# Kernel tuning notes

Measured on AMD Instinct MI355X. Metric: run time of the kernel, lower is better.

The kernel has to match this reference:

```python
import jax, jax.numpy as jnp
import numpy as np

NUM_LEVELS = 8
BASE_RES = 32
MAX_RES = 2048
FEAT_DIM = 8
MAX_TABLE = 2 ** 19
WIDTH = 256
DEPTH = 8
NUM_FREQS = 4
N = 1048576

RESOLUTIONS = [min(BASE_RES * 2 ** l, MAX_RES) for l in range(NUM_LEVELS)]
TABLE_SIZES = [min(r ** 3, MAX_TABLE) for r in RESOLUTIONS]
POS_DIM = NUM_LEVELS * FEAT_DIM            # 64
VIEW_DIM = 3 + 3 * 2 * NUM_FREQS          # 27
IN_DIM = POS_DIM + VIEW_DIM                # 91


def _xavier(key, shape):
    fan_in, fan_out = shape[-2], shape[-1]
    limit = float(np.sqrt(6.0 / (fan_in + fan_out)))
    return jax.random.uniform(key, shape, jnp.float32, -limit, limit)


def setup_inputs() -> dict:
    key = jax.random.key(0)
    ks = jax.random.split(key, 32)
    inp = {
        'positions': jax.random.uniform(ks[0], (N, 3), jnp.float32),  # in [0,1) subset of [-1,1]
        'viewdirs': jax.random.normal(ks[1], (N, 3), jnp.float32),
    }
    for l in range(NUM_LEVELS):
        inp[f'table{l}'] = _xavier(ks[2 + l], (TABLE_SIZES[l], FEAT_DIM))
    inp['w0'] = _xavier(ks[12], (IN_DIM, WIDTH))
    inp['b0'] = jnp.zeros((WIDTH,), jnp.float32)
    # 6 hidden (with ReLU) + 1 final (no ReLU) 256x256 linears, stacked
    inp['wh'] = _xavier(ks[13], (DEPTH - 1, WIDTH, WIDTH))
    inp['bh'] = jnp.zeros((DEPTH - 1, WIDTH), jnp.float32)
    inp['wd'] = _xavier(ks[14], (WIDTH, 1))
    inp['bd'] = jnp.zeros((1,), jnp.float32)
    inp['wc'] = _xavier(ks[15], (WIDTH, 3))
    inp['bc'] = jnp.zeros((3,), jnp.float32)
    return inp


def _hash_encode(positions, table, res):
    # (p + 1) * 0.5 * res, clamped to [0, res-1]
    ps = jnp.clip((positions + 1.0) * (0.5 * res), 0.0, res - 1.0)
    idx_f = ps[..., 0] * (res * res) + ps[..., 1] * res + ps[..., 2]
    # clamp in float first so int32 cast is safe (matches torch clamp-to-table)
    idx = jnp.clip(idx_f, 0.0, table.shape[0] - 1.0).astype(jnp.int32)
    return table[idx]  # [..., FEAT_DIM]


def _view_encode(v):
    feats = [v]
    for f in range(NUM_FREQS):
        feats.append(jnp.sin((2.0 ** f) * jnp.pi * v))
        feats.append(jnp.cos((2.0 ** f) * jnp.pi * v))
    return jnp.concatenate(feats, axis=-1)


def reference(positions, viewdirs, table0, table1, table2, table3, table4,
              table5, table6, table7, w0, b0, wh, bh, wd, bd, wc, bc):
    tables = [table0, table1, table2, table3, table4, table5, table6, table7]
    spatial = jnp.concatenate(
        [_hash_encode(positions, tables[l], RESOLUTIONS[l]) for l in range(NUM_LEVELS)],
        axis=-1)                                           # [N, 64]
    feats = jnp.concatenate([spatial, _view_encode(viewdirs)], axis=-1)  # [N, 91]

    x = jax.nn.relu(feats @ w0 + b0)
    for i in range(DEPTH - 2):                             # 6 hidden layers with ReLU
        x = jax.nn.relu(x @ wh[i] + bh[i])
    x = x @ wh[DEPTH - 2] + bh[DEPTH - 2]                  # final linear, no ReLU

    density = x @ wd + bd                                  # [N, 1]
    color = jax.nn.sigmoid(x @ wc + bc)                    # [N, 3]
    return density, color
```

## Files before the change

### kernel.cpp

```cpp
#include <hip/hip_runtime.h>
#include <math.h>

#define N_PTS 1048576

typedef _Float16 half8 __attribute__((ext_vector_type(8)));
typedef _Float16 half4v __attribute__((ext_vector_type(4)));
typedef float float4v __attribute__((ext_vector_type(4)));
typedef float f32x16 __attribute__((ext_vector_type(16)));

#define W0T_OFF 0
#define WHT_OFF 24576
#define WHEAD_OFF 483328
#define WS_HALVES 487424

__global__ void prep_weights(const float* __restrict__ w0,
                             const float* __restrict__ wh,
                             const float* __restrict__ wd,
                             const float* __restrict__ wc,
                             _Float16* __restrict__ ws) {
  int stride = gridDim.x * blockDim.x;
  for (int i = blockIdx.x * blockDim.x + threadIdx.x; i < WS_HALVES; i += stride) {
    float v;
    if (i < WHT_OFF) {
      int kb = i >> 11, n = (i >> 3) & 255, j = i & 7;
      int k = kb * 8 + j;
      v = (k < 91) ? w0[k * 256 + n] : 0.0f;
    } else if (i < WHEAD_OFF) {
      int rel = i - WHT_OFF;
      int layer = rel >> 16;
      int r = rel & 65535;
      int kb = r >> 11, n = (r >> 3) & 255, j = r & 7;
      int k = kb * 8 + j;
      v = wh[(layer << 16) + k * 256 + n];
    } else {
      int rel = i - WHEAD_OFF;
      int n = rel >> 8, k = rel & 255;
      v = (n == 0) ? wd[k] : ((n < 4) ? wc[k * 3 + n - 1] : 0.0f);
    }
    ws[i] = (_Float16)v;
  }
}

__device__ __forceinline__ int xaddr(int m, int kb) {
  return m * 512 + (kb ^ ((m & 7) << 4));
}

template <int KB>
__device__ __forceinline__ void mlp_layer(char* X, const _Float16* __restrict__ Wt,
                                          const float* __restrict__ bias, bool relu,
                                          int w, int lr5, int lg2) {
  f32x16 acc[4];
#pragma unroll
  for (int mt = 0; mt < 4; ++mt)
#pragma unroll
    for (int r = 0; r < 16; ++r) acc[mt][r] = 0.0f;

  const _Float16* wbase = Wt + ((size_t)(lg2 * 256 + w * 32 + lr5)) * 8;
  const int swz = (lr5 & 7) << 4;
  const int cbase = lg2 * 16;

  half8 a_cur = *(const half8*)wbase;
#pragma unroll
  for (int ks = 0; ks < KB; ++ks) {
    half8 a_nxt = a_cur;
    if (ks + 1 < KB) a_nxt = *(const half8*)(wbase + (size_t)(ks + 1) * 4096);
    const int c = (ks * 32 + cbase) ^ swz;
#pragma unroll
    for (int mt = 0; mt < 4; ++mt) {
      half8 b = *(const half8*)&X[(mt * 32 + lr5) * 512 + c];
      acc[mt] = __builtin_amdgcn_mfma_f32_32x32x16_f16(a_cur, b, acc[mt], 0, 0, 0);
    }
    a_cur = a_nxt;
  }
  __syncthreads();

  const float* bptr = bias + w * 32 + lg2 * 4;
  float4v bq[4];
#pragma unroll
  for (int q = 0; q < 4; ++q) bq[q] = *(const float4v*)(bptr + q * 8);
#pragma unroll
  for (int mt = 0; mt < 4; ++mt) {
    const int rowb = (mt * 32 + lr5) * 512;
#pragma unroll
    for (int q = 0; q < 4; ++q) {
      half4v hv;
#pragma unroll
      for (int rr = 0; rr < 4; ++rr) {
        float y = acc[mt][q * 4 + rr] + bq[q][rr];
        if (relu) y = fmaxf(y, 0.0f);
        hv[rr] = (_Float16)y;
      }
      *(half4v*)&X[rowb + ((w * 64 + q * 16 + lg2 * 8) ^ swz)] = hv;
    }
  }
  __syncthreads();
}

__global__ __launch_bounds__(512, 4) void nerf_fused(
    const float* __restrict__ pos, const float* __restrict__ vdir,
    const float* __restrict__ t0, const float* __restrict__ t1,
    const float* __restrict__ t2, const float* __restrict__ t3,
    const float* __restrict__ t4, const float* __restrict__ t5,
    const float* __restrict__ t6, const float* __restrict__ t7,
    const float* __restrict__ b0, const float* __restrict__ bh,
    const float* __restrict__ bd, const float* __restrict__ bc,
    const _Float16* __restrict__ ws, float* __restrict__ out) {
  __shared__ __align__(16) char X[65536];
  const int tid = threadIdx.x;
  const int wg = blockIdx.x;
  const int m = tid & 127;
  const int part = tid >> 7;
  const int p = wg * 128 + m;

  if (part < 3) {
    const float px = pos[p * 3], py = pos[p * 3 + 1], pz = pos[p * 3 + 2];
    const float* tabs[8] = {t0, t1, t2, t3, t4, t5, t6, t7};
    const int resi[8] = {32, 64, 128, 256, 512, 1024, 2048, 2048};
    const float tmax[8] = {32767.0f, 262143.0f, 524287.0f, 524287.0f,
                           524287.0f, 524287.0f, 524287.0f, 524287.0f};
    const int lv0 = part * 3;
    const int lv1 = (part == 2) ? 8 : lv0 + 3;
    for (int lv = lv0; lv < lv1; ++lv) {
      const float r = (float)resi[lv];
      const float hr = 0.5f * r;
      const float rm1 = r - 1.0f;
      float cx = fminf(fmaxf(__fmul_rn(__fadd_rn(px, 1.0f), hr), 0.0f), rm1);
      float cy = fminf(fmaxf(__fmul_rn(__fadd_rn(py, 1.0f), hr), 0.0f), rm1);
      float cz = fminf(fmaxf(__fmul_rn(__fadd_rn(pz, 1.0f), hr), 0.0f), rm1);
      float idxf = __fadd_rn(__fadd_rn(__fmul_rn(cx, r * r), __fmul_rn(cy, r)), cz);
      idxf = fminf(fmaxf(idxf, 0.0f), tmax[lv]);
      int idx = (int)idxf;
      const float4* row = (const float4*)(tabs[lv] + (size_t)idx * 8);
      float4 f0 = row[0], f1 = row[1];
      half8 h;
      h[0] = (_Float16)f0.x; h[1] = (_Float16)f0.y;
      h[2] = (_Float16)f0.z; h[3] = (_Float16)f0.w;
      h[4] = (_Float16)f1.x; h[5] = (_Float16)f1.y;
      h[6] = (_Float16)f1.z; h[7] = (_Float16)f1.w;
      *(half8*)&X[xaddr(m, lv * 16)] = h;
    }
  } else {
    float v0 = vdir[p * 3], v1 = vdir[p * 3 + 1], v2 = vdir[p * 3 + 2];
    const float cf[4] = {(float)(M_PI), (float)(2.0 * M_PI),
                         (float)(4.0 * M_PI), (float)(8.0 * M_PI)};
    float feat[32];
    feat[0] = v0; feat[1] = v1; feat[2] = v2;
    float vv[3] = {v0, v1, v2};
#pragma unroll
    for (int f = 0; f < 4; ++f)
#pragma unroll
      for (int d = 0; d < 3; ++d) {
        float arg = __fmul_rn(cf[f], vv[d]);
        feat[3 + f * 6 + d] = __sinf(arg);
        feat[6 + f * 6 + d] = __cosf(arg);
      }
#pragma unroll
    for (int i = 27; i < 32; ++i) feat[i] = 0.0f;
#pragma unroll
    for (int s = 0; s < 4; ++s) {
      half8 h;
#pragma unroll
      for (int j = 0; j < 8; ++j) h[j] = (_Float16)feat[s * 8 + j];
      *(half8*)&X[xaddr(m, 128 + s * 16)] = h;
    }
  }
  __syncthreads();

  const int lane = tid & 63;
  const int w = tid >> 6;
  const int lr5 = lane & 31;
  const int lg2 = lane >> 5;

  mlp_layer<6>(X, ws + W0T_OFF, b0, true, w, lr5, lg2);
#pragma unroll 1
  for (int i = 0; i < 7; ++i)
    mlp_layer<16>(X, ws + WHT_OFF + (i << 16), bh + (i << 8), i < 6, w, lr5, lg2);

  const int lr = lane & 15;
  const int lg = lane >> 4;
  float4v hacc;
  {
    float bv = (lr == 0) ? bd[0] : ((lr < 4) ? bc[lr - 1] : 0.0f);
    hacc = (float4v){bv, bv, bv, bv};
  }
  const _Float16* Wh = ws + WHEAD_OFF;
#pragma unroll
  for (int ks = 0; ks < 8; ++ks) {
    half8 bfr = *(const half8*)(Wh + lr * 256 + ks * 32 + lg * 8);
    half8 a = *(const half8*)&X[xaddr(w * 16 + lr, ks * 64 + lg * 16)];
    hacc = __builtin_amdgcn_mfma_f32_16x16x32_f16(a, bfr, hacc, 0, 0, 0);
  }
#pragma unroll
  for (int r = 0; r < 4; ++r) {
    int pp = wg * 128 + w * 16 + lg * 4 + r;
    float vv = hacc[r];
    if (lr == 0) {
      out[pp] = vv;
    } else if (lr < 4) {
      out[N_PTS + 3 * pp + (lr - 1)] = 1.0f / (1.0f + __expf(-vv));
    }
  }
}

extern "C" void kernel_launch(void* const* d_in, const int* in_sizes, int n_in,
                              void* d_out, int out_size, void* d_ws, size_t ws_size,
                              hipStream_t stream) {
  const float* pos = (const float*)d_in[0];
  const float* vdir = (const float*)d_in[1];
  const float* t0 = (const float*)d_in[2];
  const float* t1 = (const float*)d_in[3];
  const float* t2 = (const float*)d_in[4];
  const float* t3 = (const float*)d_in[5];
  const float* t4 = (const float*)d_in[6];
  const float* t5 = (const float*)d_in[7];
  const float* t6 = (const float*)d_in[8];
  const float* t7 = (const float*)d_in[9];
  const float* w0 = (const float*)d_in[10];
  const float* b0 = (const float*)d_in[11];
  const float* wh = (const float*)d_in[12];
  const float* bh = (const float*)d_in[13];
  const float* wd = (const float*)d_in[14];
  const float* bd = (const float*)d_in[15];
  const float* wc = (const float*)d_in[16];
  const float* bc = (const float*)d_in[17];
  _Float16* ws = (_Float16*)d_ws;
  float* out = (float*)d_out;

  hipLaunchKernelGGL(prep_weights, dim3((WS_HALVES + 255) / 256), dim3(256), 0, stream,
                     w0, wh, wd, wc, ws);
  hipLaunchKernelGGL(nerf_fused, dim3(N_PTS / 128), dim3(512), 0, stream,
                     pos, vdir, t0, t1, t2, t3, t4, t5, t6, t7,
                     b0, bh, bd, bc, (const _Float16*)ws, out);
}
```

Before: 983.4 us.

## Halve block to 4 waves, each computing 64 output columns for reuse

Cuts the workgroup from 8 to 4 waves. Each wave now computes two 32-wide N tiles, so each B fragment loaded from LDS feeds two MFMAs, halving LDS reads per MFMA. Bias is folded into the accumulator initialisation and the head now handles 32 rows per wave. The cost is twice the accumulator registers (128 fp32 per thread), fewer waves to hide latency, and the hash gather now done by only 128 threads per block.

```diff
diff --git a/kernel.cpp b/kernel.cpp
--- a/kernel.cpp
+++ b/kernel.cpp
@@ -49,54 +49,66 @@
 __device__ __forceinline__ void mlp_layer(char* X, const _Float16* __restrict__ Wt,
                                           const float* __restrict__ bias, bool relu,
                                           int w, int lr5, int lg2) {
-  f32x16 acc[4];
-#pragma unroll
-  for (int mt = 0; mt < 4; ++mt)
-#pragma unroll
-    for (int r = 0; r < 16; ++r) acc[mt][r] = 0.0f;
-
-  const _Float16* wbase = Wt + ((size_t)(lg2 * 256 + w * 32 + lr5)) * 8;
+  f32x16 acc[2][4];
+#pragma unroll
+  for (int nt = 0; nt < 2; ++nt)
+#pragma unroll
+    for (int q = 0; q < 4; ++q) {
+      float4v bv = *(const float4v*)(bias + w * 64 + nt * 32 + q * 8 + lg2 * 4);
+#pragma unroll
+      for (int mt = 0; mt < 4; ++mt)
+#pragma unroll
+        for (int rr = 0; rr < 4; ++rr) acc[nt][mt][q * 4 + rr] = bv[rr];
+    }
+
+  const _Float16* wbase = Wt + ((size_t)(lg2 * 256 + w * 64 + lr5)) * 8;
   const int swz = (lr5 & 7) << 4;
   const int cbase = lg2 * 16;
 
-  half8 a_cur = *(const half8*)wbase;
+  half8 a0 = *(const half8*)wbase;
+  half8 a1 = *(const half8*)(wbase + 256);
 #pragma unroll
   for (int ks = 0; ks < KB; ++ks) {
-    half8 a_nxt = a_cur;
-    if (ks + 1 < KB) a_nxt = *(const half8*)(wbase + (size_t)(ks + 1) * 4096);
+    half8 a0n = a0, a1n = a1;
+    if (ks + 1 < KB) {
+      a0n = *(const half8*)(wbase + (size_t)(ks + 1) * 4096);
+      a1n = *(const half8*)(wbase + (size_t)(ks + 1) * 4096 + 256);
+    }
     const int c = (ks * 32 + cbase) ^ swz;
+    half8 b[4];
+#pragma unroll
+    for (int mt = 0; mt < 4; ++mt) b[mt] = *(const half8*)&X[(mt * 32 + lr5) * 512 + c];
 #pragma unroll
     for (int mt = 0; mt < 4; ++mt) {
-      half8 b = *(const half8*)&X[(mt * 32 + lr5) * 512 + c];
-      acc[mt] = __builtin_amdgcn_mfma_f32_32x32x16_f16(a_cur, b, acc[mt], 0, 0, 0);
-    }
-    a_cur = a_nxt;
+      acc[0][mt] = __builtin_amdgcn_mfma_f32_32x32x16_f16(a0, b[mt], acc[0][mt], 0, 0, 0);
+      acc[1][mt] = __builtin_amdgcn_mfma_f32_32x32x16_f16(a1, b[mt], acc[1][mt], 0, 0, 0);
+    }
+    a0 = a0n;
+    a1 = a1n;
   }
   __syncthreads();
 
-  const float* bptr = bias + w * 32 + lg2 * 4;
-  float4v bq[4];
-#pragma unroll
-  for (int q = 0; q < 4; ++q) bq[q] = *(const float4v*)(bptr + q * 8);
 #pragma unroll
   for (int mt = 0; mt < 4; ++mt) {
     const int rowb = (mt * 32 + lr5) * 512;
 #pragma unroll
-    for (int q = 0; q < 4; ++q) {
-      half4v hv;
-#pragma unroll
-      for (int rr = 0; rr < 4; ++rr) {
-        float y = acc[mt][q * 4 + rr] + bq[q][rr];
-        if (relu) y = fmaxf(y, 0.0f);
-        hv[rr] = (_Float16)y;
+    for (int nt = 0; nt < 2; ++nt)
+#pragma unroll
+      for (int q = 0; q < 4; ++q) {
+        half4v hv;
+#pragma unroll
+        for (int rr = 0; rr < 4; ++rr) {
+          float y = acc[nt][mt][q * 4 + rr];
+          if (relu) y = fmaxf(y, 0.0f);
+          hv[rr] = (_Float16)y;
+        }
+        *(half4v*)&X[rowb + ((w * 128 + nt * 64 + q * 16 + lg2 * 8) ^ swz)] = hv;
       }
-      *(half4v*)&X[rowb + ((w * 64 + q * 16 + lg2 * 8) ^ swz)] = hv;
-    }
   }
   __syncthreads();
 }
 
-__global__ __launch_bounds__(512, 4) void nerf_fused(
+__global__ __launch_bounds__(256, 2) void nerf_fused(
     const float* __restrict__ pos, const float* __restrict__ vdir,
     const float* __restrict__ t0, const float* __restrict__ t1,
     const float* __restrict__ t2, const float* __restrict__ t3,
@@ -109,18 +121,16 @@
   const int tid = threadIdx.x;
   const int wg = blockIdx.x;
   const int m = tid & 127;
-  const int part = tid >> 7;
   const int p = wg * 128 + m;
 
-  if (part < 3) {
+  if (tid < 128) {
     const float px = pos[p * 3], py = pos[p * 3 + 1], pz = pos[p * 3 + 2];
     const float* tabs[8] = {t0, t1, t2, t3, t4, t5, t6, t7};
     const int resi[8] = {32, 64, 128, 256, 512, 1024, 2048, 2048};
     const float tmax[8] = {32767.0f, 262143.0f, 524287.0f, 524287.0f,
                            524287.0f, 524287.0f, 524287.0f, 524287.0f};
-    const int lv0 = part * 3;
-    const int lv1 = (part == 2) ? 8 : lv0 + 3;
-    for (int lv = lv0; lv < lv1; ++lv) {
+#pragma unroll
+    for (int lv = 0; lv < 8; ++lv) {
       const float r = (float)resi[lv];
       const float hr = 0.5f * r;
       const float rm1 = r - 1.0f;
@@ -178,28 +188,34 @@
 
   const int lr = lane & 15;
   const int lg = lane >> 4;
-  float4v hacc;
+  float4v hacc[2];
   {
     float bv = (lr == 0) ? bd[0] : ((lr < 4) ? bc[lr - 1] : 0.0f);
-    hacc = (float4v){bv, bv, bv, bv};
+    hacc[0] = (float4v){bv, bv, bv, bv};
+    hacc[1] = hacc[0];
   }
   const _Float16* Wh = ws + WHEAD_OFF;
 #pragma unroll
   for (int ks = 0; ks < 8; ++ks) {
     half8 bfr = *(const half8*)(Wh + lr * 256 + ks * 32 + lg * 8);
-    half8 a = *(const half8*)&X[xaddr(w * 16 + lr, ks * 64 + lg * 16)];
-    hacc = __builtin_amdgcn_mfma_f32_16x16x32_f16(a, bfr, hacc, 0, 0, 0);
-  }
-#pragma unroll
-  for (int r = 0; r < 4; ++r) {
-    int pp = wg * 128 + w * 16 + lg * 4 + r;
-    float vv = hacc[r];
-    if (lr == 0) {
-      out[pp] = vv;
-    } else if (lr < 4) {
-      out[N_PTS + 3 * pp + (lr - 1)] = 1.0f / (1.0f + __expf(-vv));
-    }
-  }
+#pragma unroll
+    for (int mt = 0; mt < 2; ++mt) {
+      half8 a = *(const half8*)&X[xaddr(w * 32 + mt * 16 + lr, ks * 64 + lg * 16)];
+      hacc[mt] = __builtin_amdgcn_mfma_f32_16x16x32_f16(a, bfr, hacc[mt], 0, 0, 0);
+    }
+  }
+#pragma unroll
+  for (int mt = 0; mt < 2; ++mt)
+#pragma unroll
+    for (int r = 0; r < 4; ++r) {
+      int pp = wg * 128 + w * 32 + mt * 16 + lg * 4 + r;
+      float vv = hacc[mt][r];
+      if (lr == 0) {
+        out[pp] = vv;
+      } else if (lr < 4) {
+        out[N_PTS + 3 * pp + (lr - 1)] = 1.0f / (1.0f + __expf(-vv));
+      }
+    }
 }
 
 extern "C" void kernel_launch(void* const* d_in, const int* in_sizes, int n_in,
@@ -228,7 +244,7 @@
 
   hipLaunchKernelGGL(prep_weights, dim3((WS_HALVES + 255) / 256), dim3(256), 0, stream,
                      w0, wh, wd, wc, ws);
-  hipLaunchKernelGGL(nerf_fused, dim3(N_PTS / 128), dim3(512), 0, stream,
+  hipLaunchKernelGGL(nerf_fused, dim3(N_PTS / 128), dim3(256), 0, stream,
                      pos, vdir, t0, t1, t2, t3, t4, t5, t6, t7,
                      b0, bh, bd, bc, (const _Float16*)ws, out);
 }
```

After: 1.003 ms. 1.02x slower.

## Retile MLP layers into 2x2 MFMA warp tiles with cross-layer weight prefetch

Applied to the files above, without the earlier changes.

Each wave now computes a 64-output by 64-point tile (2x2 32x32 MFMA blocks) instead of 32 outputs by all 128 points. This halves the LDS activation reads per MFMA and loads two weight fragments per k-step. The first weight fragment of the next layer is prefetched during the last k-step of the current one, and bias is folded into the accumulator initialisation. The LDS swizzle widens from 8 to 16 rows to match the new access pattern. The trade-off is higher register pressure and a read of the head weights as a dummy prefetch after the last layer.

```diff
diff --git a/kernel.cpp b/kernel.cpp
--- a/kernel.cpp
+++ b/kernel.cpp
@@ -42,56 +42,67 @@
 }
 
 __device__ __forceinline__ int xaddr(int m, int kb) {
-  return m * 512 + (kb ^ ((m & 7) << 4));
+  return m * 512 + (kb ^ ((m & 15) << 4));
 }
 
 template <int KB>
 __device__ __forceinline__ void mlp_layer(char* X, const _Float16* __restrict__ Wt,
+                                          const _Float16* __restrict__ Wt_next,
+                                          size_t laneoff,
                                           const float* __restrict__ bias, bool relu,
-                                          int w, int lr5, int lg2) {
-  f32x16 acc[4];
-#pragma unroll
-  for (int mt = 0; mt < 4; ++mt)
-#pragma unroll
-    for (int r = 0; r < 16; ++r) acc[mt][r] = 0.0f;
-
-  const _Float16* wbase = Wt + ((size_t)(lg2 * 256 + w * 32 + lr5)) * 8;
-  const int swz = (lr5 & 7) << 4;
+                                          int wn, int wm, int lr5, int lg2,
+                                          half8& a0, half8& a1) {
+  f32x16 acc[2][2];
+#pragma unroll
+  for (int nt = 0; nt < 2; ++nt)
+#pragma unroll
+    for (int q = 0; q < 4; ++q) {
+      float4v bv = *(const float4v*)(bias + wn * 64 + nt * 32 + q * 8 + lg2 * 4);
+#pragma unroll
+      for (int mt = 0; mt < 2; ++mt)
+#pragma unroll
+        for (int rr = 0; rr < 4; ++rr) acc[nt][mt][q * 4 + rr] = bv[rr];
+    }
+
+  const _Float16* wb = Wt + laneoff;
+  const _Float16* wbn = Wt_next + laneoff;
+  const int swz = (lr5 & 15) << 4;
   const int cbase = lg2 * 16;
-
-  half8 a_cur = *(const half8*)wbase;
+  const int row0 = (wm * 64 + lr5) * 512;
+
 #pragma unroll
   for (int ks = 0; ks < KB; ++ks) {
-    half8 a_nxt = a_cur;
-    if (ks + 1 < KB) a_nxt = *(const half8*)(wbase + (size_t)(ks + 1) * 4096);
+    const _Float16* nb = (ks + 1 < KB) ? (wb + (size_t)(ks + 1) * 4096) : wbn;
+    half8 a0n = *(const half8*)nb;
+    half8 a1n = *(const half8*)(nb + 256);
     const int c = (ks * 32 + cbase) ^ swz;
-#pragma unroll
-    for (int mt = 0; mt < 4; ++mt) {
-      half8 b = *(const half8*)&X[(mt * 32 + lr5) * 512 + c];
-      acc[mt] = __builtin_amdgcn_mfma_f32_32x32x16_f16(a_cur, b, acc[mt], 0, 0, 0);
-    }
-    a_cur = a_nxt;
+    half8 b0 = *(const half8*)&X[row0 + c];
+    half8 b1 = *(const half8*)&X[row0 + 32 * 512 + c];
+    acc[0][0] = __builtin_amdgcn_mfma_f32_32x32x16_f16(a0, b0, acc[0][0], 0, 0, 0);
+    acc[0][1] = __builtin_amdgcn_mfma_f32_32x32x16_f16(a0, b1, acc[0][1], 0, 0, 0);
+    acc[1][0] = __builtin_amdgcn_mfma_f32_32x32x16_f16(a1, b0, acc[1][0], 0, 0, 0);
+    acc[1][1] = __builtin_amdgcn_mfma_f32_32x32x16_f16(a1, b1, acc[1][1], 0, 0, 0);
+    a0 = a0n;
+    a1 = a1n;
   }
   __syncthreads();
 
-  const float* bptr = bias + w * 32 + lg2 * 4;
-  float4v bq[4];
-#pragma unroll
-  for (int q = 0; q < 4; ++q) bq[q] = *(const float4v*)(bptr + q * 8);
-#pragma unroll
-  for (int mt = 0; mt < 4; ++mt) {
-    const int rowb = (mt * 32 + lr5) * 512;
-#pragma unroll
-    for (int q = 0; q < 4; ++q) {
-      half4v hv;
-#pragma unroll
-      for (int rr = 0; rr < 4; ++rr) {
-        float y = acc[mt][q * 4 + rr] + bq[q][rr];
-        if (relu) y = fmaxf(y, 0.0f);
-        hv[rr] = (_Float16)y;
+#pragma unroll
+  for (int mt = 0; mt < 2; ++mt) {
+    const int rowb = (wm * 64 + mt * 32 + lr5) * 512;
+#pragma unroll
+    for (int nt = 0; nt < 2; ++nt)
+#pragma unroll
+      for (int q = 0; q < 4; ++q) {
+        half4v hv;
+#pragma unroll
+        for (int rr = 0; rr < 4; ++rr) {
+          float y = acc[nt][mt][q * 4 + rr];
+          if (relu) y = fmaxf(y, 0.0f);
+          hv[rr] = (_Float16)y;
+        }
+        *(half4v*)&X[rowb + ((wn * 128 + nt * 64 + q * 16 + lg2 * 8) ^ swz)] = hv;
       }
-      *(half4v*)&X[rowb + ((w * 64 + q * 16 + lg2 * 8) ^ swz)] = hv;
-    }
   }
   __syncthreads();
 }
@@ -164,17 +175,28 @@
       *(half8*)&X[xaddr(m, 128 + s * 16)] = h;
     }
   }
-  __syncthreads();
 
   const int lane = tid & 63;
   const int w = tid >> 6;
+  const int wn = w & 3;
+  const int wm = w >> 2;
   const int lr5 = lane & 31;
   const int lg2 = lane >> 5;
-
-  mlp_layer<6>(X, ws + W0T_OFF, b0, true, w, lr5, lg2);
+  const size_t laneoff = ((size_t)(lg2 * 256 + wn * 64 + lr5)) * 8;
+
+  half8 a0 = *(const half8*)(ws + W0T_OFF + laneoff);
+  half8 a1 = *(const half8*)(ws + W0T_OFF + laneoff + 256);
+  __syncthreads();
+
+  mlp_layer<6>(X, ws + W0T_OFF, ws + WHT_OFF, laneoff, b0, true,
+               wn, wm, lr5, lg2, a0, a1);
 #pragma unroll 1
-  for (int i = 0; i < 7; ++i)
-    mlp_layer<16>(X, ws + WHT_OFF + (i << 16), bh + (i << 8), i < 6, w, lr5, lg2);
+  for (int i = 0; i < 7; ++i) {
+    const _Float16* wnext =
+        (i < 6) ? (ws + WHT_OFF + ((i + 1) << 16)) : (ws + WHEAD_OFF);
+    mlp_layer<16>(X, ws + WHT_OFF + (i << 16), wnext, laneoff, bh + (i << 8),
+                  i < 6, wn, wm, lr5, lg2, a0, a1);
+  }
 
   const int lr = lane & 15;
   const int lg = lane >> 4;
```

Result: slower. 1.156 ms (+17.5%).
